# Kernel optimization log

Hardware: AMD Instinct MI355X
Metric: run time of the kernel (lower is better)

Reference implementation:

```python
import math
import jax, jax.numpy as jnp
import numpy as np

N_QUBITS = 16
BATCH = 128
N_STATE = 2 ** N_QUBITS


def cnot_ring(n_qubits):
    """Permutation equivalent to a CNOT ring (faithful copy of the torch repo's numpy code)."""
    n2 = np.array([0, 2, 3, 1])
    if n_qubits == 2:
        return n2
    evens = np.zeros(2 ** (n_qubits - 1))
    answer = n2[::2]
    for i in range(1, n_qubits - 1):
        evens[:2 ** i] = answer
        a, b = np.array_split(answer, 2)
        evens[2 ** i:2 ** i + 2 ** (i - 1)] = a + 3 * 2 ** i
        evens[2 ** i + 2 ** (i - 1):2 ** (i + 1)] = b + 2 ** i
        answer = evens[:2 ** (i + 1)]
    a, b = np.split(evens.copy() + 2 ** (n_qubits - 2), 2)
    a = np.mod(a, 2 ** (n_qubits - 1))
    b, c = np.split(b, 2)
    b = b - 2 ** (n_qubits - 1)
    odds = np.concatenate((a, b, c), axis=0)[::-1]
    output = np.zeros(2 ** n_qubits)
    output[::2] = evens
    output[1::2] = odds
    return output.astype(int)


def binary_mask(n_qubits):
    """[n, 2**n] matrix; row i is bit (n-1-i from LSB) of the column index,
    matching torch binary_matrix (dim 0 of the [2]*n tensor is the MSB)."""
    idx = jnp.arange(2 ** n_qubits, dtype=jnp.int32)
    shifts = (n_qubits - 1 - jnp.arange(n_qubits, dtype=jnp.int32))
    return ((idx[None, :] >> shifts[:, None]) & 1).astype(jnp.float32)


def wht(x):
    """Walsh-Hadamard transform over the last dim of [B, N] complex state (had_big butterfly)."""
    B, N = x.shape
    n = int(math.log2(N))
    for i in range(n):
        x = x.reshape(B, 2 ** i, 2, N >> (i + 1))
        a, b = x[:, :, 0, :], x[:, :, 1, :]
        x = jnp.stack([a + b, a - b], axis=2)
    return x.reshape(B, N) * jnp.asarray(2.0 ** (-n / 2), dtype=x.dtype)


def setup_inputs() -> dict:
    key = jax.random.key(0)
    k1, k2, k3 = jax.random.split(key, 3)
    state_re = jax.random.normal(k1, (BATCH, N_STATE), dtype=jnp.float32)
    state_im = jax.random.normal(k2, (BATCH, N_STATE), dtype=jnp.float32)
    thetas = jax.random.normal(k3, (BATCH, N_QUBITS), dtype=jnp.float32)
    cnot_p = jnp.asarray(cnot_ring(N_QUBITS), dtype=jnp.int32)
    return {"state_re": state_re, "state_im": state_im, "thetas": thetas, "cnot_p": cnot_p}


def reference(state_re, state_im, thetas, cnot_p):
    # set_state('random'): l2-normalize complex state per batch row
    norm = jnp.sqrt(jnp.sum(state_re * state_re + state_im * state_im, axis=-1, keepdims=True))
    state = (state_re + 1j * state_im) / norm  # complex64 [B, N]
    # hadamard layer (had_big WHT butterfly)
    state = wht(state)
    # RZ layer: thetas @ binary mask -> phase eigenvalues exp(-i*theta/2)
    ang = thetas @ binary_mask(N_QUBITS)  # [B, N]
    state = state * jnp.exp(-0.5j * ang)
    # CNOT ring: gather permutation over the state axis
    state = state[:, cnot_p]
    # second hadamard layer
    state = wht(state)
    # measure(): probabilities |psi|^2
    return jnp.abs(state) ** 2
```

## Files before the change

kernel.cpp:

```cpp
#include <hip/hip_runtime.h>

#define NB 128
#define NS 65536

typedef float v2f __attribute__((ext_vector_type(2)));

__device__ __forceinline__ v2f pk_fma(v2f a, v2f b, v2f c) {
  v2f d;
  asm("v_pk_fma_f32 %0, %1, %2, %3" : "=v"(d) : "v"(a), "v"(b), "v"(c));
  return d;
}
__device__ __forceinline__ v2f pk_add(v2f a, v2f b) {
  v2f d;
  asm("v_pk_add_f32 %0, %1, %2" : "=v"(d) : "v"(a), "v"(b));
  return d;
}
__device__ __forceinline__ v2f pk_mul(v2f a, v2f b) {
  v2f d;
  asm("v_pk_mul_f32 %0, %1, %2" : "=v"(d) : "v"(a), "v"(b));
  return d;
}

template <int CTRL>
__device__ __forceinline__ float dppmov(float x) {
  return __int_as_float(__builtin_amdgcn_update_dpp(
      0, __float_as_int(x), CTRL, 0xF, 0xF, false));
}
__device__ __forceinline__ float xor4mov(float x) {
  int t = __builtin_amdgcn_update_dpp(0, __float_as_int(x), 0x104, 0xF, 0x5, false);
  t = __builtin_amdgcn_update_dpp(t, __float_as_int(x), 0x114, 0xF, 0xA, false);
  return __int_as_float(t);
}

__device__ __forceinline__ void wht256p(v2f (&p)[4], int lane) {
  const v2f M1 = {-1.f, -1.f};
  {
    v2f t;
    t = p[0]; p[0] = pk_add(t, p[1]); p[1] = pk_fma(M1, p[1], t);
    t = p[2]; p[2] = pk_add(t, p[3]); p[3] = pk_fma(M1, p[3], t);
    t = p[0]; p[0] = pk_add(t, p[2]); p[2] = pk_fma(M1, p[2], t);
    t = p[1]; p[1] = pk_add(t, p[3]); p[3] = pk_fma(M1, p[3], t);
  }
  const float s1f  = (lane & 1)  ? -1.f : 1.f;
  const float s2f  = (lane & 2)  ? -1.f : 1.f;
  const float s4f  = (lane & 4)  ? -1.f : 1.f;
  const float s8f  = (lane & 8)  ? -1.f : 1.f;
  const float s16f = (lane & 16) ? -1.f : 1.f;
  const float s32f = (lane & 32) ? -1.f : 1.f;
  const v2f s1 = {s1f, s1f}, s2 = {s2f, s2f}, s4 = {s4f, s4f};
  const v2f s8 = {s8f, s8f}, s16 = {s16f, s16f}, s32 = {s32f, s32f};
#pragma unroll
  for (int q = 0; q < 4; ++q) {
    v2f m = {dppmov<0xB1>(p[q].x), dppmov<0xB1>(p[q].y)};
    p[q] = pk_fma(s1, p[q], m);
  }
#pragma unroll
  for (int q = 0; q < 4; ++q) {
    v2f m = {dppmov<0x4E>(p[q].x), dppmov<0x4E>(p[q].y)};
    p[q] = pk_fma(s2, p[q], m);
  }
#pragma unroll
  for (int q = 0; q < 4; ++q) {
    v2f m = {xor4mov(p[q].x), xor4mov(p[q].y)};
    p[q] = pk_fma(s4, p[q], m);
  }
#pragma unroll
  for (int q = 0; q < 4; ++q) {
    v2f m = {dppmov<0x128>(p[q].x), dppmov<0x128>(p[q].y)};
    p[q] = pk_fma(s8, p[q], m);
  }
#pragma unroll
  for (int q = 0; q < 4; ++q) {
    auto rre = __builtin_amdgcn_permlane16_swap(__float_as_uint(p[q].x),
                                                __float_as_uint(p[q].x), false, false);
    auto rim = __builtin_amdgcn_permlane16_swap(__float_as_uint(p[q].y),
                                                __float_as_uint(p[q].y), false, false);
    v2f lo = {__uint_as_float(rre[0]), __uint_as_float(rim[0])};
    v2f hi = {__uint_as_float(rre[1]), __uint_as_float(rim[1])};
    p[q] = pk_fma(s16, hi, lo);
  }
#pragma unroll
  for (int q = 0; q < 4; ++q) {
    auto rre = __builtin_amdgcn_permlane32_swap(__float_as_uint(p[q].x),
                                                __float_as_uint(p[q].x), false, false);
    auto rim = __builtin_amdgcn_permlane32_swap(__float_as_uint(p[q].y),
                                                __float_as_uint(p[q].y), false, false);
    v2f lo = {__uint_as_float(rre[0]), __uint_as_float(rim[0])};
    v2f hi = {__uint_as_float(rre[1]), __uint_as_float(rim[1])};
    p[q] = pk_fma(s32, hi, lo);
  }
}

__global__ __launch_bounds__(1024, 8) void k1_ahi(const float* __restrict__ sre,
                                                  const float* __restrict__ sim,
                                                  const float* __restrict__ thetas,
                                                  float* __restrict__ T,
                                                  float* __restrict__ partial) {
  __shared__ float sr[32][260];
  __shared__ float si[32][260];
  __shared__ float2 phh4[64];
  __shared__ float2 phHQ[4];
  __shared__ float red[16];
  const int bid = blockIdx.x;
  const int b = bid >> 2, qd = bid & 3;
  const int lo0 = qd * 64, lo1 = lo0 + 32;
  const int tid = threadIdx.x, lane = tid & 63, w = tid >> 6;
  const float* pre = sre + ((size_t)b << 16);
  const float* pim = sim + ((size_t)b << 16);
  const int c = tid & 7, jr = tid >> 3;
  const int j0 = jr, j1 = jr + 128;
  const float4 vr0 = *reinterpret_cast<const float4*>(pre + j0 * 256 + lo0 + c * 4);
  const float4 vi0 = *reinterpret_cast<const float4*>(pim + j0 * 256 + lo0 + c * 4);
  const float4 vr1 = *reinterpret_cast<const float4*>(pre + j1 * 256 + lo0 + c * 4);
  const float4 vi1 = *reinterpret_cast<const float4*>(pim + j1 * 256 + lo0 + c * 4);
  const float4 wr0 = *reinterpret_cast<const float4*>(pre + j0 * 256 + lo1 + c * 4);
  const float4 wi0 = *reinterpret_cast<const float4*>(pim + j0 * 256 + lo1 + c * 4);
  const float4 wr1 = *reinterpret_cast<const float4*>(pre + j1 * 256 + lo1 + c * 4);
  const float4 wi1 = *reinterpret_cast<const float4*>(pim + j1 * 256 + lo1 + c * 4);
  if (tid < 64) {
    const float* tb = thetas + b * 16;
    float a = 0.f;
#pragma unroll
    for (int i = 0; i < 6; ++i)
      if ((tid >> (5 - i)) & 1) a += tb[i];
    phh4[tid] = make_float2(cosf(0.5f * a), -sinf(0.5f * a));
    if (tid < 4) {
      float aq = 0.f;
      if (tid & 1) aq += tb[7];
      if (tid & 2) aq += tb[6];
      phHQ[tid] = make_float2(cosf(0.5f * aq), -sinf(0.5f * aq));
    }
  }
  v2f acc2 = {0.f, 0.f};
#define ACC4(f) do { \
    v2f u0 = {f.x, f.y}, u1 = {f.z, f.w}; \
    acc2 = pk_fma(u0, u0, acc2); acc2 = pk_fma(u1, u1, acc2); } while (0)
  ACC4(vr0); ACC4(vi0); ACC4(vr1); ACC4(vi1);
  ACC4(wr0); ACC4(wi0); ACC4(wr1); ACC4(wi1);
#undef ACC4
  float acc = acc2.x + acc2.y;
#pragma unroll
  for (int m2 = 32; m2 >= 1; m2 >>= 1) acc += __shfl_xor(acc, m2, 64);
  if (lane == 0) red[w] = acc;
  const int fs = ((c >> 1) & 3) << 2;
  const int j0s = j0 ^ fs, j1s = j1 ^ fs;
  sr[c*4+0][j0s] = vr0.x; sr[c*4+1][j0s] = vr0.y; sr[c*4+2][j0s] = vr0.z; sr[c*4+3][j0s] = vr0.w;
  si[c*4+0][j0s] = vi0.x; si[c*4+1][j0s] = vi0.y; si[c*4+2][j0s] = vi0.z; si[c*4+3][j0s] = vi0.w;
  sr[c*4+0][j1s] = vr1.x; sr[c*4+1][j1s] = vr1.y; sr[c*4+2][j1s] = vr1.z; sr[c*4+3][j1s] = vr1.w;
  si[c*4+0][j1s] = vi1.x; si[c*4+1][j1s] = vi1.y; si[c*4+2][j1s] = vi1.z; si[c*4+3][j1s] = vi1.w;
  __syncthreads();
  if (tid == 0) {
    float sm = 0.f;
#pragma unroll
    for (int k = 0; k < 16; ++k) sm += red[k];
    partial[bid] = sm;
  }
  const float2 p4 = phh4[lane];
  float prq[4], piq[4];
#pragma unroll
  for (int q = 0; q < 4; ++q) {
    const float2 pq = phHQ[q];
    prq[q] = p4.x * pq.x - p4.y * pq.y;
    piq[q] = p4.x * pq.y + p4.y * pq.x;
  }
  float* Tb = T + ((size_t)b << 17);
  const int mrow = tid >> 2, sub = tid & 3;
#pragma unroll
  for (int t = 0; t < 2; ++t) {
#pragma unroll
    for (int r = 0; r < 2; ++r) {
      const int ll = w * 2 + r;
      const int blk = lane ^ ((ll >> 3) & 3);
      const float4 a4 = *reinterpret_cast<const float4*>(&sr[ll][blk * 4]);
      const float4 b4 = *reinterpret_cast<const float4*>(&si[ll][blk * 4]);
      v2f p[4] = {{a4.x, b4.x}, {a4.y, b4.y}, {a4.z, b4.z}, {a4.w, b4.w}};
      wht256p(p, lane);
#pragma unroll
      for (int q = 0; q < 4; ++q) {
        const float ur = p[q].x, ui = p[q].y;
        const v2f tt = pk_mul(p[q], (v2f){prq[q], prq[q]});
        p[q].x = fmaf(-piq[q], ui, tt.x);
        p[q].y = fmaf(piq[q], ur, tt.y);
      }
      wht256p(p, lane);
      *reinterpret_cast<float4*>(&sr[ll][blk * 4]) =
          make_float4(p[0].x, p[1].x, p[2].x, p[3].x);
      *reinterpret_cast<float4*>(&si[ll][blk * 4]) =
          make_float4(p[0].y, p[1].y, p[2].y, p[3].y);
    }
    __syncthreads();
    float* dst = Tb + ((size_t)mrow << 9) + (size_t)(t == 0 ? lo0 : lo1) * 2;
#pragma unroll
    for (int j = 0; j < 4; ++j) {
      const int l0 = 8 * j + 2 * sub;
      const int ms = mrow ^ ((j & 3) << 2);
      *reinterpret_cast<float4*>(dst + l0 * 2) =
          make_float4(sr[l0][ms], si[l0][ms], sr[l0 + 1][ms], si[l0 + 1][ms]);
    }
    if (t == 0) {
      __syncthreads();
      sr[c*4+0][j0s] = wr0.x; sr[c*4+1][j0s] = wr0.y; sr[c*4+2][j0s] = wr0.z; sr[c*4+3][j0s] = wr0.w;
      si[c*4+0][j0s] = wi0.x; si[c*4+1][j0s] = wi0.y; si[c*4+2][j0s] = wi0.z; si[c*4+3][j0s] = wi0.w;
      sr[c*4+0][j1s] = wr1.x; sr[c*4+1][j1s] = wr1.y; sr[c*4+2][j1s] = wr1.z; sr[c*4+3][j1s] = wr1.w;
      si[c*4+0][j1s] = wi1.x; si[c*4+1][j1s] = wi1.y; si[c*4+2][j1s] = wi1.z; si[c*4+3][j1s] = wi1.w;
      __syncthreads();
    }
  }
}

__global__ __launch_bounds__(256, 8) void k2_alo_scatter(const float* __restrict__ T,
                                                         const float* __restrict__ thetas,
                                                         const int* __restrict__ cnot,
                                                         const float* __restrict__ partial,
                                                         float* __restrict__ outp) {
  __shared__ float2 phl4[64];
  __shared__ float2 phLQ[4];
  __shared__ int sloL[64];
  __shared__ int tj[16];
  __shared__ int srow16[16];
  __shared__ float th[16];
  __shared__ float shinv;
  const int bid = blockIdx.x;
  const int x = bid & 7, s2i = bid >> 3;
  const int b = x * 16 + (s2i >> 4), tile = s2i & 15;
  const int tid = threadIdx.x, lane = tid & 63, w = tid >> 6;
  if (tid < 16) {
    th[tid] = thetas[b * 16 + tid];
    int v = 0;
#pragma unroll
    for (int i = 0; i < 16; ++i) v |= ((cnot[1 << i] >> tid) & 1) << i;
    tj[tid] = v;
  }
  if (tid == 0) {
    float sum = 0.f;
#pragma unroll
    for (int k = 0; k < 4; ++k) sum += partial[b * 4 + k];
    shinv = 1.0f / (sum * 4294967296.0f);
  }
  __syncthreads();
  if (tid < 64) {
    float a = 0.f;
#pragma unroll
    for (int i = 0; i < 6; ++i)
      if ((tid >> (5 - i)) & 1) a += th[8 + i];
    phl4[tid] = make_float2(cosf(0.5f * a), -sinf(0.5f * a));
    int v = 0;
#pragma unroll
    for (int bb = 0; bb < 6; ++bb)
      if ((tid >> bb) & 1) v ^= tj[2 + bb];
    sloL[tid] = v;
    if (tid < 4) {
      float aq = 0.f;
      if (tid & 1) aq += th[15];
      if (tid & 2) aq += th[14];
      phLQ[tid] = make_float2(cosf(0.5f * aq), -sinf(0.5f * aq));
    }
  }
  if (tid < 16) {
    const int mh = tile * 16 + tid;
    int v = 0;
#pragma unroll
    for (int bb = 0; bb < 8; ++bb)
      if ((mh >> bb) & 1) v ^= tj[8 + bb];
    srow16[tid] = v;
  }
  __syncthreads();
  const float* Tb = T + ((size_t)b << 17);
  float* ob = outp + ((size_t)b << 16);
  const float iv = shinv;
  const float2 p4 = phl4[lane];
  const int sL = sloL[lane];
  const int sq1 = tj[0], sq2 = tj[1], sq3 = tj[0] ^ tj[1];
  float prq[4], piq[4];
#pragma unroll
  for (int q = 0; q < 4; ++q) {
    const float2 pq = phLQ[q];
    prq[q] = p4.x * pq.x - p4.y * pq.y;
    piq[q] = p4.x * pq.y + p4.y * pq.x;
  }
  const float* rbase = Tb + ((size_t)(tile * 16 + w * 4) << 9) + lane * 8;
#define LDROW(A, B, r) \
  const float4 A = *reinterpret_cast<const float4*>(rbase + (r) * 512); \
  const float4 B = *reinterpret_cast<const float4*>(rbase + (r) * 512 + 4)
#define PROC(A, B, r) do { \
    v2f p[4] = {{A.x, A.y}, {A.z, A.w}, {B.x, B.y}, {B.z, B.w}}; \
    wht256p(p, lane); \
    _Pragma("unroll") \
    for (int q = 0; q < 4; ++q) { \
      const float ur = p[q].x, ui = p[q].y; \
      const v2f tt = pk_mul(p[q], (v2f){prq[q], prq[q]}); \
      p[q].x = fmaf(-piq[q], ui, tt.x); \
      p[q].y = fmaf(piq[q], ur, tt.y); \
    } \
    wht256p(p, lane); \
    const int base = srow16[w * 4 + (r)] ^ sL; \
    const v2f m0 = pk_mul(p[0], p[0]); \
    const v2f m1 = pk_mul(p[1], p[1]); \
    const v2f m2 = pk_mul(p[2], p[2]); \
    const v2f m3 = pk_mul(p[3], p[3]); \
    ob[base]       = (m0.x + m0.y) * iv; \
    ob[base ^ sq1] = (m1.x + m1.y) * iv; \
    ob[base ^ sq2] = (m2.x + m2.y) * iv; \
    ob[base ^ sq3] = (m3.x + m3.y) * iv; } while (0)
  LDROW(A0, B0, 0);
  LDROW(A1, B1, 1);
  LDROW(A2, B2, 2);
  PROC(A0, B0, 0);
  LDROW(A3, B3, 3);
  PROC(A1, B1, 1);
  PROC(A2, B2, 2);
  PROC(A3, B3, 3);
#undef LDROW
#undef PROC
}

extern "C" void kernel_launch(void* const* d_in, const int* in_sizes, int n_in,
                              void* d_out, int out_size, void* d_ws, size_t ws_size,
                              hipStream_t stream) {
  const float* sre = (const float*)d_in[0];
  const float* sim = (const float*)d_in[1];
  const float* thetas = (const float*)d_in[2];
  const int* cnot = (const int*)d_in[3];
  float* outp = (float*)d_out;
  char* w = (char*)d_ws;
  const size_t CPLANE = (size_t)NB * NS * 2 * sizeof(float);
  if (ws_size < CPLANE + 8192) return;
  float* T = (float*)(w);
  float* partial = (float*)(w + CPLANE);

  hipLaunchKernelGGL(k1_ahi, dim3(512), dim3(1024), 0, stream, sre, sim, thetas, T, partial);
  hipLaunchKernelGGL(k2_alo_scatter, dim3(2048), dim3(256), 0, stream, T, thetas, cnot, partial, outp);
}
```

Baseline: 70.66 us.

## Split k1 into smaller 16-column tiles with 512-thread blocks

k1 now processes one 16-column tile per block: 512 threads and a grid of 2048 blocks, replacing 1024-thread blocks that each handled two 32-column halves in sequence. This removes the two-pass loop and its extra barriers, cuts shared memory per block, and gives more blocks to spread across CUs. The XOR swizzle on LDS accesses is dropped, so transposed reads may hit bank conflicts. Global stores now write 64 bytes contiguously per row instead of larger chunks, and k2 has to sum 16 partial norms per batch row instead of 4.

After: 71.82 us. About the same (+1.6%).

```diff
diff --git a/kernel.cpp b/kernel.cpp
--- a/kernel.cpp
+++ b/kernel.cpp
@@ -91,32 +91,20 @@
   }
 }
 
-__global__ __launch_bounds__(1024, 8) void k1_ahi(const float* __restrict__ sre,
-                                                  const float* __restrict__ sim,
-                                                  const float* __restrict__ thetas,
-                                                  float* __restrict__ T,
-                                                  float* __restrict__ partial) {
-  __shared__ float sr[32][260];
-  __shared__ float si[32][260];
+__global__ __launch_bounds__(512, 8) void k1_ahi(const float* __restrict__ sre,
+                                                 const float* __restrict__ sim,
+                                                 const float* __restrict__ thetas,
+                                                 float* __restrict__ T,
+                                                 float* __restrict__ partial) {
+  __shared__ float sr[16][260];
+  __shared__ float si[16][260];
   __shared__ float2 phh4[64];
   __shared__ float2 phHQ[4];
-  __shared__ float red[16];
+  __shared__ float red[8];
   const int bid = blockIdx.x;
-  const int b = bid >> 2, qd = bid & 3;
-  const int lo0 = qd * 64, lo1 = lo0 + 32;
+  const int b = bid >> 4, tile = bid & 15;
+  const int lo0 = tile * 16;
   const int tid = threadIdx.x, lane = tid & 63, w = tid >> 6;
-  const float* pre = sre + ((size_t)b << 16);
-  const float* pim = sim + ((size_t)b << 16);
-  const int c = tid & 7, jr = tid >> 3;
-  const int j0 = jr, j1 = jr + 128;
-  const float4 vr0 = *reinterpret_cast<const float4*>(pre + j0 * 256 + lo0 + c * 4);
-  const float4 vi0 = *reinterpret_cast<const float4*>(pim + j0 * 256 + lo0 + c * 4);
-  const float4 vr1 = *reinterpret_cast<const float4*>(pre + j1 * 256 + lo0 + c * 4);
-  const float4 vi1 = *reinterpret_cast<const float4*>(pim + j1 * 256 + lo0 + c * 4);
-  const float4 wr0 = *reinterpret_cast<const float4*>(pre + j0 * 256 + lo1 + c * 4);
-  const float4 wi0 = *reinterpret_cast<const float4*>(pim + j0 * 256 + lo1 + c * 4);
-  const float4 wr1 = *reinterpret_cast<const float4*>(pre + j1 * 256 + lo1 + c * 4);
-  const float4 wi1 = *reinterpret_cast<const float4*>(pim + j1 * 256 + lo1 + c * 4);
   if (tid < 64) {
     const float* tb = thetas + b * 16;
     float a = 0.f;
@@ -131,28 +119,33 @@
       phHQ[tid] = make_float2(cosf(0.5f * aq), -sinf(0.5f * aq));
     }
   }
+  const float* pre = sre + ((size_t)b << 16);
+  const float* pim = sim + ((size_t)b << 16);
+  const int c = tid & 3, jr = tid >> 2;
+  const int j0 = jr, j1 = jr + 128;
+  const float4 vr0 = *reinterpret_cast<const float4*>(pre + j0 * 256 + lo0 + c * 4);
+  const float4 vi0 = *reinterpret_cast<const float4*>(pim + j0 * 256 + lo0 + c * 4);
+  const float4 vr1 = *reinterpret_cast<const float4*>(pre + j1 * 256 + lo0 + c * 4);
+  const float4 vi1 = *reinterpret_cast<const float4*>(pim + j1 * 256 + lo0 + c * 4);
   v2f acc2 = {0.f, 0.f};
 #define ACC4(f) do { \
     v2f u0 = {f.x, f.y}, u1 = {f.z, f.w}; \
     acc2 = pk_fma(u0, u0, acc2); acc2 = pk_fma(u1, u1, acc2); } while (0)
   ACC4(vr0); ACC4(vi0); ACC4(vr1); ACC4(vi1);
-  ACC4(wr0); ACC4(wi0); ACC4(wr1); ACC4(wi1);
 #undef ACC4
+  sr[c*4+0][j0] = vr0.x; sr[c*4+1][j0] = vr0.y; sr[c*4+2][j0] = vr0.z; sr[c*4+3][j0] = vr0.w;
+  si[c*4+0][j0] = vi0.x; si[c*4+1][j0] = vi0.y; si[c*4+2][j0] = vi0.z; si[c*4+3][j0] = vi0.w;
+  sr[c*4+0][j1] = vr1.x; sr[c*4+1][j1] = vr1.y; sr[c*4+2][j1] = vr1.z; sr[c*4+3][j1] = vr1.w;
+  si[c*4+0][j1] = vi1.x; si[c*4+1][j1] = vi1.y; si[c*4+2][j1] = vi1.z; si[c*4+3][j1] = vi1.w;
   float acc = acc2.x + acc2.y;
 #pragma unroll
   for (int m2 = 32; m2 >= 1; m2 >>= 1) acc += __shfl_xor(acc, m2, 64);
   if (lane == 0) red[w] = acc;
-  const int fs = ((c >> 1) & 3) << 2;
-  const int j0s = j0 ^ fs, j1s = j1 ^ fs;
-  sr[c*4+0][j0s] = vr0.x; sr[c*4+1][j0s] = vr0.y; sr[c*4+2][j0s] = vr0.z; sr[c*4+3][j0s] = vr0.w;
-  si[c*4+0][j0s] = vi0.x; si[c*4+1][j0s] = vi0.y; si[c*4+2][j0s] = vi0.z; si[c*4+3][j0s] = vi0.w;
-  sr[c*4+0][j1s] = vr1.x; sr[c*4+1][j1s] = vr1.y; sr[c*4+2][j1s] = vr1.z; sr[c*4+3][j1s] = vr1.w;
-  si[c*4+0][j1s] = vi1.x; si[c*4+1][j1s] = vi1.y; si[c*4+2][j1s] = vi1.z; si[c*4+3][j1s] = vi1.w;
   __syncthreads();
   if (tid == 0) {
     float sm = 0.f;
 #pragma unroll
-    for (int k = 0; k < 16; ++k) sm += red[k];
+    for (int k = 0; k < 8; ++k) sm += red[k];
     partial[bid] = sm;
   }
   const float2 p4 = phh4[lane];
@@ -163,48 +156,35 @@
     prq[q] = p4.x * pq.x - p4.y * pq.y;
     piq[q] = p4.x * pq.y + p4.y * pq.x;
   }
+#pragma unroll
+  for (int r = 0; r < 2; ++r) {
+    const int ll = w * 2 + r;
+    const float4 a4 = *reinterpret_cast<const float4*>(&sr[ll][lane * 4]);
+    const float4 b4 = *reinterpret_cast<const float4*>(&si[ll][lane * 4]);
+    v2f p[4] = {{a4.x, b4.x}, {a4.y, b4.y}, {a4.z, b4.z}, {a4.w, b4.w}};
+    wht256p(p, lane);
+#pragma unroll
+    for (int q = 0; q < 4; ++q) {
+      const float ur = p[q].x, ui = p[q].y;
+      const v2f tt = pk_mul(p[q], (v2f){prq[q], prq[q]});
+      p[q].x = fmaf(-piq[q], ui, tt.x);
+      p[q].y = fmaf(piq[q], ur, tt.y);
+    }
+    wht256p(p, lane);
+    *reinterpret_cast<float4*>(&sr[ll][lane * 4]) =
+        make_float4(p[0].x, p[1].x, p[2].x, p[3].x);
+    *reinterpret_cast<float4*>(&si[ll][lane * 4]) =
+        make_float4(p[0].y, p[1].y, p[2].y, p[3].y);
+  }
+  __syncthreads();
   float* Tb = T + ((size_t)b << 17);
-  const int mrow = tid >> 2, sub = tid & 3;
-#pragma unroll
-  for (int t = 0; t < 2; ++t) {
-#pragma unroll
-    for (int r = 0; r < 2; ++r) {
-      const int ll = w * 2 + r;
-      const int blk = lane ^ ((ll >> 3) & 3);
-      const float4 a4 = *reinterpret_cast<const float4*>(&sr[ll][blk * 4]);
-      const float4 b4 = *reinterpret_cast<const float4*>(&si[ll][blk * 4]);
-      v2f p[4] = {{a4.x, b4.x}, {a4.y, b4.y}, {a4.z, b4.z}, {a4.w, b4.w}};
-      wht256p(p, lane);
-#pragma unroll
-      for (int q = 0; q < 4; ++q) {
-        const float ur = p[q].x, ui = p[q].y;
-        const v2f tt = pk_mul(p[q], (v2f){prq[q], prq[q]});
-        p[q].x = fmaf(-piq[q], ui, tt.x);
-        p[q].y = fmaf(piq[q], ur, tt.y);
-      }
-      wht256p(p, lane);
-      *reinterpret_cast<float4*>(&sr[ll][blk * 4]) =
-          make_float4(p[0].x, p[1].x, p[2].x, p[3].x);
-      *reinterpret_cast<float4*>(&si[ll][blk * 4]) =
-          make_float4(p[0].y, p[1].y, p[2].y, p[3].y);
-    }
-    __syncthreads();
-    float* dst = Tb + ((size_t)mrow << 9) + (size_t)(t == 0 ? lo0 : lo1) * 2;
-#pragma unroll
-    for (int j = 0; j < 4; ++j) {
-      const int l0 = 8 * j + 2 * sub;
-      const int ms = mrow ^ ((j & 3) << 2);
-      *reinterpret_cast<float4*>(dst + l0 * 2) =
-          make_float4(sr[l0][ms], si[l0][ms], sr[l0 + 1][ms], si[l0 + 1][ms]);
-    }
-    if (t == 0) {
-      __syncthreads();
-      sr[c*4+0][j0s] = wr0.x; sr[c*4+1][j0s] = wr0.y; sr[c*4+2][j0s] = wr0.z; sr[c*4+3][j0s] = wr0.w;
-      si[c*4+0][j0s] = wi0.x; si[c*4+1][j0s] = wi0.y; si[c*4+2][j0s] = wi0.z; si[c*4+3][j0s] = wi0.w;
-      sr[c*4+0][j1s] = wr1.x; sr[c*4+1][j1s] = wr1.y; sr[c*4+2][j1s] = wr1.z; sr[c*4+3][j1s] = wr1.w;
-      si[c*4+0][j1s] = wi1.x; si[c*4+1][j1s] = wi1.y; si[c*4+2][j1s] = wi1.z; si[c*4+3][j1s] = wi1.w;
-      __syncthreads();
-    }
+  const int m = tid >> 1, L = (tid & 1) * 8;
+  float* dst = Tb + ((size_t)m << 9) + (size_t)(lo0 + L) * 2;
+#pragma unroll
+  for (int j = 0; j < 4; ++j) {
+    const int l0 = L + 2 * j;
+    *reinterpret_cast<float4*>(dst + j * 4) =
+        make_float4(sr[l0][m], si[l0][m], sr[l0 + 1][m], si[l0 + 1][m]);
   }
 }
 
@@ -234,7 +214,7 @@
   if (tid == 0) {
     float sum = 0.f;
 #pragma unroll
-    for (int k = 0; k < 4; ++k) sum += partial[b * 4 + k];
+    for (int k = 0; k < 16; ++k) sum += partial[b * 16 + k];
     shinv = 1.0f / (sum * 4294967296.0f);
   }
   __syncthreads();
@@ -324,10 +304,10 @@
   float* outp = (float*)d_out;
   char* w = (char*)d_ws;
   const size_t CPLANE = (size_t)NB * NS * 2 * sizeof(float);
-  if (ws_size < CPLANE + 8192) return;
+  if (ws_size < CPLANE + 16384) return;
   float* T = (float*)(w);
   float* partial = (float*)(w + CPLANE);
 
-  hipLaunchKernelGGL(k1_ahi, dim3(512), dim3(1024), 0, stream, sre, sim, thetas, T, partial);
+  hipLaunchKernelGGL(k1_ahi, dim3(2048), dim3(512), 0, stream, sre, sim, thetas, T, partial);
   hipLaunchKernelGGL(k2_alo_scatter, dim3(2048), dim3(256), 0, stream, T, thetas, cnot, partial, outp);
 }
```
